# Optimization experiments

Measured on AMD Instinct MI355X. Metric: run time of the kernel, lower is better.

The kernel has to match this reference:

```python
import math
import jax, jax.numpy as jnp
import numpy as np

B, N, D, H = 4, 2048, 512, 8
HD = D // H


def setup_inputs() -> dict:
    key = jax.random.key(0)
    ks = jax.random.split(key, 7)
    w_scale = 1.0 / math.sqrt(D)  # keep logits in a sane range (like default init)
    return {
        "q": jax.random.normal(ks[0], (B, N, D), dtype=jnp.float32),
        "mask": jax.random.randint(ks[1], (B, N), 0, 2) == 1,  # True = masked key
        "attn_bias": jax.random.normal(ks[2], (B, N, N), dtype=jnp.float32),
        "Wq": jax.random.normal(ks[3], (D, D), dtype=jnp.float32) * w_scale,
        "Wk": jax.random.normal(ks[4], (D, D), dtype=jnp.float32) * w_scale,
        "Wv": jax.random.normal(ks[5], (D, D), dtype=jnp.float32) * w_scale,
        "Wo": jax.random.normal(ks[6], (D, D), dtype=jnp.float32) * w_scale,
    }


def _heads(v):
    # [B, N, D] -> [H, B, N, HD]  (mirrors reshape + movedim(-2, 0))
    b, n, d = v.shape
    return v.reshape(b, n, H, HD).transpose(2, 0, 1, 3)


def reference(q, mask, attn_bias, Wq, Wk, Wv, Wo):
    # Linear projections (torch Linear: x @ W.T)
    qh = _heads(q @ Wq.T)
    kh = _heads(q @ Wk.T)   # self-attention: h defaults to q
    vh = _heads(q @ Wv.T)
    # scores: [H, B, Nq, Nk]
    scores = jnp.einsum("hbqd,hbkd->hbqk", qh, kh) / math.sqrt(HD)
    scores = scores + attn_bias[None]                     # broadcast over heads
    scores = jnp.where(mask[None, :, None, :], -jnp.inf, scores)
    attn = jax.nn.softmax(scores, axis=-1)
    out = jnp.einsum("hbqk,hbkd->hbqd", attn, vh)         # [H, B, Nq, HD]
    out = out.transpose(1, 2, 0, 3).reshape(q.shape[0], q.shape[1], D)
    return out @ Wo.T
```

## Files before the change

kernel.cpp:

```cpp
#include <hip/hip_runtime.h>
#include <stdint.h>


typedef __attribute__((ext_vector_type(8))) short short8;
typedef __attribute__((ext_vector_type(4))) short short4v;
typedef __attribute__((ext_vector_type(4))) float f32x4;

#define DEV static __device__ __forceinline__

constexpr int Bc = 4, Nc = 2048, Dc = 512, Hc = 8, HDc = 64;
constexpr int Mc = Bc * Nc;
constexpr int QKVNc = 3 * Dc;

DEV unsigned short f2bits(float f) {
  union { float f; unsigned u; } a; a.f = f;
  unsigned r = a.u + 0x7fffu + ((a.u >> 16) & 1u);
  return (unsigned short)(r >> 16);
}
DEV unsigned pack_bf16x2(float a, float b) {
  unsigned ua = __float_as_uint(a), ub = __float_as_uint(b);
  ua = ua + 0x7fffu + ((ua >> 16) & 1u);
  ub = ub + 0x7fffu + ((ub >> 16) & 1u);
  return __builtin_amdgcn_perm(ub, ua, 0x07060302);
}
DEV unsigned pack_shorts(short a, short b) {
  return (unsigned)(unsigned short)a | ((unsigned)(unsigned short)b << 16);
}

__global__ void cvt_kernel(const float* __restrict__ src, short* __restrict__ dst, int n4) {
  int i = blockIdx.x * blockDim.x + threadIdx.x;
  if (i >= n4) return;
  float4 v = ((const float4*)src)[i];
  short4v o = { (short)f2bits(v.x), (short)f2bits(v.y), (short)f2bits(v.z), (short)f2bits(v.w) };
  ((short4v*)dst)[i] = o;
}

__global__ void detect_kernel(const uchar4* __restrict__ m, int* __restrict__ flag) {
  __shared__ int s;
  if (threadIdx.x == 0) s = 0;
  __syncthreads();
  int acc = 0;
  for (int i = threadIdx.x; i < (Bc * Nc) / 4; i += 256) {
    uchar4 v = m[i];
    acc |= (int)v.y | (int)v.z | (int)v.w;
  }
  if (acc) atomicOr(&s, 1);
  __syncthreads();
  if (threadIdx.x == 0) *flag = s;
}

__global__ void mask_kernel(const void* __restrict__ mask, const int* __restrict__ flag,
                            float* __restrict__ mf, int n) {
  int i = blockIdx.x * blockDim.x + threadIdx.x;
  if (i >= n) return;
  int isbyte = *flag;
  int v = isbyte ? (int)((const unsigned char*)mask)[i] : ((const int*)mask)[i];
  mf[i] = v ? -1e30f : 0.0f;
}

template<bool OUT_F32>
__global__ __launch_bounds__(256) void gemm_bt(const short* __restrict__ A,
                                               const short* __restrict__ Bm,
                                               void* __restrict__ Cv,
                                               int M, int N, int K,
                                               int qcols, float cscale) {
  __shared__ __align__(16) short At[128 * 72];
  __shared__ __align__(16) short Bt[128 * 72];
  const int tid = threadIdx.x, lane = tid & 63, wv = tid >> 6;
  const int quad = lane >> 4, l16 = lane & 15;
  const int mbase = blockIdx.y * 128, nbase = blockIdx.x * 128;
  const int wr = (wv >> 1) * 64, wc = (wv & 1) * 64;
  const float scale = (nbase < qcols) ? cscale : 1.0f;
  const int srow = tid >> 1, sch8 = (tid & 1) * 32;
  (void)srow; (void)sch8;
  f32x4 acc[4][4] = {};
  short8 apre[4], bpre[4];
#pragma unroll
  for (int i = 0; i < 4; i++) {
    int flat = i * 256 + tid, row = flat >> 3, ch8 = (flat & 7) * 8;
    apre[i] = *(const short8*)&A[(size_t)(mbase + row) * K + ch8];
    bpre[i] = *(const short8*)&Bm[(size_t)(nbase + row) * K + ch8];
  }
  for (int k0 = 0; k0 < K; k0 += 64) {
    __syncthreads();
#pragma unroll
    for (int i = 0; i < 4; i++) {
      int flat = i * 256 + tid, row = flat >> 3, ch8 = (flat & 7) * 8;
      *(short8*)&At[row * 72 + ch8] = apre[i];
      *(short8*)&Bt[row * 72 + ch8] = bpre[i];
    }
    if (k0 + 64 < K) {
#pragma unroll
      for (int i = 0; i < 4; i++) {
        int flat = i * 256 + tid, row = flat >> 3, ch8 = (flat & 7) * 8;
        apre[i] = *(const short8*)&A[(size_t)(mbase + row) * K + k0 + 64 + ch8];
        bpre[i] = *(const short8*)&Bm[(size_t)(nbase + row) * K + k0 + 64 + ch8];
      }
    }
    __syncthreads();
#pragma unroll
    for (int s = 0; s < 2; s++) {
      short8 af[4], bf[4];
#pragma unroll
      for (int t = 0; t < 4; t++) {
        af[t] = *(short8*)&At[(wr + t * 16 + l16) * 72 + quad * 8 + s * 32];
        bf[t] = *(short8*)&Bt[(wc + t * 16 + l16) * 72 + quad * 8 + s * 32];
      }
#pragma unroll
      for (int mt = 0; mt < 4; mt++)
#pragma unroll
        for (int nt = 0; nt < 4; nt++)
          acc[mt][nt] = __builtin_amdgcn_mfma_f32_16x16x32_bf16(af[mt], bf[nt], acc[mt][nt], 0, 0, 0);
    }
  }
#pragma unroll
  for (int mt = 0; mt < 4; mt++)
#pragma unroll
    for (int nt = 0; nt < 4; nt++)
#pragma unroll
      for (int r = 0; r < 4; r++) {
        int row = mbase + wr + mt * 16 + quad * 4 + r;
        int col = nbase + wc + nt * 16 + l16;
        float v = acc[mt][nt][r] * scale;
        if (OUT_F32) ((float*)Cv)[(size_t)row * N + col] = v;
        else         ((short*)Cv)[(size_t)row * N + col] = (short)f2bits(v);
      }
}

__global__ __launch_bounds__(256) void attn_kernel(const short* __restrict__ QKV,
                                                   const float* __restrict__ bias,
                                                   const float* __restrict__ maskf,
                                                   short* __restrict__ Aout) {
  __shared__ __align__(16) short Kt[64 * 72];
  __shared__ __align__(16) short Vt[64 * 72];
  __shared__ __align__(16) short Pt[4][16 * 72];
  __shared__ __align__(16) float mlds[Nc];
  __shared__ float lred[4][16];
  const int tid = threadIdx.x, lane = tid & 63, wv = tid >> 6;
  const int quad = lane >> 4, l16 = lane & 15;
  const int qt = blockIdx.x & 31, h = (blockIdx.x >> 5) & 7, b = (int)(blockIdx.x >> 8);
  const int qrow0 = qt * 64;
  const int qglob = qrow0 + wv * 16 + l16;
  const float* biasrow = bias + ((size_t)b * Nc + qglob) * Nc;
  const float* mfb = maskf + b * Nc;

  ((float4*)mlds)[tid]       = ((const float4*)mfb)[tid];
  ((float4*)mlds)[256 + tid] = ((const float4*)mfb)[256 + tid];

  short8 qf[2];
  {
    const short* qp = QKV + (size_t)(b * Nc + qglob) * QKVNc + h * HDc + quad * 8;
    qf[0] = *(const short8*)qp;
    qf[1] = *(const short8*)(qp + 32);
  }

  const int vp = tid & 31, vg = tid >> 5;
  const short* Kbase = QKV + Dc + h * HDc;
  const short* Vbase = QKV + 2 * Dc + h * HDc;

  short8 kpre[2], v0pre, v1pre;
  float4 bpre[4];
#pragma unroll
  for (int i = 0; i < 2; i++) {
    int flat = i * 256 + tid, row = flat >> 3, ch8 = (flat & 7) * 8;
    kpre[i] = *(const short8*)&Kbase[(size_t)(b * Nc + row) * QKVNc + ch8];
  }
  v0pre = *(const short8*)&Vbase[(size_t)(b * Nc + 2 * vp) * QKVNc + vg * 8];
  v1pre = *(const short8*)&Vbase[(size_t)(b * Nc + 2 * vp + 1) * QKVNc + vg * 8];
#pragma unroll
  for (int t = 0; t < 4; t++) bpre[t] = *(const float4*)&biasrow[t * 16 + quad * 4];

  f32x4 oacc[4] = {};
  float lsum = 0.f;

  for (int kt = 0; kt < 32; kt++) {
    const int kb = kt * 64;
    const int kbn = ((kt + 1) & 31) * 64;
    __syncthreads();
#pragma unroll
    for (int i = 0; i < 2; i++) {
      int flat = i * 256 + tid, row = flat >> 3, ch8 = (flat & 7) * 8;
      *(short8*)&Kt[row * 72 + ch8] = kpre[i];
    }
#pragma unroll
    for (int j = 0; j < 8; j++)
      *(unsigned*)&Vt[(vg * 8 + j) * 72 + 2 * vp] = pack_shorts(v0pre[j], v1pre[j]);

    float4 bcur[4];
#pragma unroll
    for (int t = 0; t < 4; t++) bcur[t] = bpre[t];
#pragma unroll
    for (int i = 0; i < 2; i++) {
      int flat = i * 256 + tid, row = flat >> 3, ch8 = (flat & 7) * 8;
      kpre[i] = *(const short8*)&Kbase[(size_t)(b * Nc + kbn + row) * QKVNc + ch8];
    }
    v0pre = *(const short8*)&Vbase[(size_t)(b * Nc + kbn + 2 * vp) * QKVNc + vg * 8];
    v1pre = *(const short8*)&Vbase[(size_t)(b * Nc + kbn + 2 * vp + 1) * QKVNc + vg * 8];
#pragma unroll
    for (int t = 0; t < 4; t++) bpre[t] = *(const float4*)&biasrow[kbn + t * 16 + quad * 4];
    __syncthreads();

    f32x4 sacc[4] = {};
#pragma unroll
    for (int s = 0; s < 2; s++)
#pragma unroll
      for (int t = 0; t < 4; t++) {
        short8 kf = *(short8*)&Kt[(t * 16 + l16) * 72 + quad * 8 + s * 32];
        sacc[t] = __builtin_amdgcn_mfma_f32_16x16x32_bf16(kf, qf[s], sacc[t], 0, 0, 0);
      }

#pragma unroll
    for (int t = 0; t < 4; t++) {
      float4 mv = *(const float4*)&mlds[kb + t * 16 + quad * 4];
      float p0 = __expf(sacc[t][0] + mv.x + bcur[t].x);
      float p1 = __expf(sacc[t][1] + mv.y + bcur[t].y);
      float p2 = __expf(sacc[t][2] + mv.z + bcur[t].z);
      float p3 = __expf(sacc[t][3] + mv.w + bcur[t].w);
      lsum += (p0 + p1) + (p2 + p3);
      uint2 u = { pack_bf16x2(p0, p1), pack_bf16x2(p2, p3) };
      *(uint2*)&Pt[wv][l16 * 72 + t * 16 + quad * 4] = u;
    }

#pragma unroll
    for (int s = 0; s < 2; s++) {
      short8 pf = *(short8*)&Pt[wv][l16 * 72 + quad * 8 + s * 32];
#pragma unroll
      for (int t = 0; t < 4; t++) {
        short8 vf = *(short8*)&Vt[(t * 16 + l16) * 72 + quad * 8 + s * 32];
        oacc[t] = __builtin_amdgcn_mfma_f32_16x16x32_bf16(pf, vf, oacc[t], 0, 0, 0);
      }
    }
  }

  lsum += __shfl_xor(lsum, 16);
  lsum += __shfl_xor(lsum, 32);
  if (quad == 0) lred[wv][l16] = lsum;
#pragma unroll
  for (int r = 0; r < 4; r++) {
    float inv = 1.0f / lred[wv][quad * 4 + r];
    int row = b * Nc + qrow0 + wv * 16 + quad * 4 + r;
#pragma unroll
    for (int t = 0; t < 4; t++)
      Aout[(size_t)row * Dc + h * HDc + t * 16 + l16] = (short)f2bits(oacc[t][r] * inv);
  }
}

extern "C" void kernel_launch(void* const* d_in, const int* in_sizes, int n_in,
                              void* d_out, int out_size, void* d_ws, size_t ws_size,
                              hipStream_t stream) {
  const float* q    = (const float*)d_in[0];
  const void*  mask = d_in[1];
  const float* bias = (const float*)d_in[2];
  const float* Wq   = (const float*)d_in[3];
  const float* Wk   = (const float*)d_in[4];
  const float* Wv   = (const float*)d_in[5];
  const float* Wo   = (const float*)d_in[6];
  float* out = (float*)d_out;

  char* ws = (char*)d_ws;
  short* qb   = (short*)ws;  ws += (size_t)Mc * Dc * 2;
  short* Wqkv = (short*)ws;  ws += (size_t)QKVNc * Dc * 2;
  short* Wob  = (short*)ws;  ws += (size_t)Dc * Dc * 2;
  float* mf   = (float*)ws;  ws += (size_t)Bc * Nc * 4;
  int*   mflag= (int*)ws;    ws += 256;
  short* QKV  = (short*)ws;  ws += (size_t)Mc * QKVNc * 2;
  short* aout = (short*)ws;  ws += (size_t)Mc * Dc * 2;

  auto cvt = [&](const float* s, short* d, int n) {
    int n4 = n >> 2;
    cvt_kernel<<<dim3((n4 + 255) / 256), dim3(256), 0, stream>>>(s, d, n4);
  };
  cvt(q, qb, Mc * Dc);
  cvt(Wq, Wqkv,               Dc * Dc);
  cvt(Wk, Wqkv + Dc * Dc,     Dc * Dc);
  cvt(Wv, Wqkv + 2 * Dc * Dc, Dc * Dc);
  cvt(Wo, Wob, Dc * Dc);
  detect_kernel<<<dim3(1), dim3(256), 0, stream>>>((const uchar4*)mask, mflag);
  mask_kernel<<<dim3((Bc * Nc + 255) / 256), dim3(256), 0, stream>>>(mask, mflag, mf, Bc * Nc);

  gemm_bt<false><<<dim3(QKVNc / 128, Mc / 128), dim3(256), 0, stream>>>(
      qb, Wqkv, (void*)QKV, Mc, QKVNc, Dc, Dc, 0.125f);
  attn_kernel<<<dim3(Bc * Hc * 32), dim3(256), 0, stream>>>(QKV, bias, mf, aout);
  gemm_bt<true><<<dim3(Dc / 128, Mc / 128), dim3(256), 0, stream>>>(
      aout, Wob, (void*)out, Mc, Dc, Dc, 0, 1.0f);
}
```

Baseline: 270.1 us.

## Fuse input conversion into QKV GEMM, merge prep kernels, enlarge attention tiles

The QKV GEMM now reads the fp32 input directly and converts it to bf16 while staging into LDS. This removes the separate conversion kernel and its intermediate buffer. The four weight-conversion launches become one kernel, and the mask detect and mask expand kernels become a single-block kernel, cutting launch count. The attention kernel now uses 512 threads with 128 query rows per block, so each K/V tile loaded into LDS serves twice as many queries. The trade-off is higher register and LDS use per block and fewer blocks in flight.

After: 263.4 us. 1.03x faster.

```diff
diff --git a/kernel.cpp b/kernel.cpp
--- a/kernel.cpp
+++ b/kernel.cpp
@@ -26,44 +26,50 @@
 DEV unsigned pack_shorts(short a, short b) {
   return (unsigned)(unsigned short)a | ((unsigned)(unsigned short)b << 16);
 }
-
-__global__ void cvt_kernel(const float* __restrict__ src, short* __restrict__ dst, int n4) {
-  int i = blockIdx.x * blockDim.x + threadIdx.x;
-  if (i >= n4) return;
-  float4 v = ((const float4*)src)[i];
+DEV short8 cvt8(float4 a, float4 b) {
+  union { short8 s; uint4 u; } r;
+  r.u.x = pack_bf16x2(a.x, a.y); r.u.y = pack_bf16x2(a.z, a.w);
+  r.u.z = pack_bf16x2(b.x, b.y); r.u.w = pack_bf16x2(b.z, b.w);
+  return r.s;
+}
+
+__global__ void cvtw_kernel(const float* __restrict__ Wq, const float* __restrict__ Wk,
+                            const float* __restrict__ Wv, const float* __restrict__ Wo,
+                            short* __restrict__ Wqkv, short* __restrict__ Wob) {
+  int which = blockIdx.x >> 8;
+  int j = (blockIdx.x & 255) * 256 + threadIdx.x;
+  const float* src = which == 0 ? Wq : which == 1 ? Wk : which == 2 ? Wv : Wo;
+  short* dst = (which == 3) ? Wob : Wqkv + which * (Dc * Dc);
+  float4 v = ((const float4*)src)[j];
   short4v o = { (short)f2bits(v.x), (short)f2bits(v.y), (short)f2bits(v.z), (short)f2bits(v.w) };
-  ((short4v*)dst)[i] = o;
-}
-
-__global__ void detect_kernel(const uchar4* __restrict__ m, int* __restrict__ flag) {
-  __shared__ int s;
-  if (threadIdx.x == 0) s = 0;
+  ((short4v*)dst)[j] = o;
+}
+
+__global__ void maskprep_kernel(const void* __restrict__ mask, float* __restrict__ mf) {
+  __shared__ int flag;
+  if (threadIdx.x == 0) flag = 0;
   __syncthreads();
+  const uchar4* m4 = (const uchar4*)mask;
   int acc = 0;
-  for (int i = threadIdx.x; i < (Bc * Nc) / 4; i += 256) {
-    uchar4 v = m[i];
+  for (int i = threadIdx.x; i < 2048; i += 1024) {
+    uchar4 v = m4[i];
     acc |= (int)v.y | (int)v.z | (int)v.w;
   }
-  if (acc) atomicOr(&s, 1);
+  if (acc) atomicOr(&flag, 1);
   __syncthreads();
-  if (threadIdx.x == 0) *flag = s;
-}
-
-__global__ void mask_kernel(const void* __restrict__ mask, const int* __restrict__ flag,
-                            float* __restrict__ mf, int n) {
-  int i = blockIdx.x * blockDim.x + threadIdx.x;
-  if (i >= n) return;
-  int isbyte = *flag;
-  int v = isbyte ? (int)((const unsigned char*)mask)[i] : ((const int*)mask)[i];
-  mf[i] = v ? -1e30f : 0.0f;
-}
-
-template<bool OUT_F32>
-__global__ __launch_bounds__(256) void gemm_bt(const short* __restrict__ A,
-                                               const short* __restrict__ Bm,
-                                               void* __restrict__ Cv,
-                                               int M, int N, int K,
-                                               int qcols, float cscale) {
+  int isbyte = flag;
+  for (int i = threadIdx.x; i < Bc * Nc; i += 1024) {
+    int v = isbyte ? (int)((const unsigned char*)mask)[i] : ((const int*)mask)[i];
+    mf[i] = v ? -1e30f : 0.0f;
+  }
+}
+
+template<bool A_F32, bool OUT_F32>
+__global__ __launch_bounds__(256, 2) void gemm_bt(const void* __restrict__ Av,
+                                                  const short* __restrict__ Bm,
+                                                  void* __restrict__ Cv,
+                                                  int M, int N, int K,
+                                                  int qcols, float cscale) {
   __shared__ __align__(16) short At[128 * 72];
   __shared__ __align__(16) short Bt[128 * 72];
   const int tid = threadIdx.x, lane = tid & 63, wv = tid >> 6;
@@ -71,14 +77,18 @@
   const int mbase = blockIdx.y * 128, nbase = blockIdx.x * 128;
   const int wr = (wv >> 1) * 64, wc = (wv & 1) * 64;
   const float scale = (nbase < qcols) ? cscale : 1.0f;
-  const int srow = tid >> 1, sch8 = (tid & 1) * 32;
-  (void)srow; (void)sch8;
   f32x4 acc[4][4] = {};
-  short8 apre[4], bpre[4];
+  float4 apf[4][2]; short8 aph[4], bpre[4];
 #pragma unroll
   for (int i = 0; i < 4; i++) {
     int flat = i * 256 + tid, row = flat >> 3, ch8 = (flat & 7) * 8;
-    apre[i] = *(const short8*)&A[(size_t)(mbase + row) * K + ch8];
+    if (A_F32) {
+      const float* Af = (const float*)Av;
+      apf[i][0] = *(const float4*)&Af[(size_t)(mbase + row) * K + ch8];
+      apf[i][1] = *(const float4*)&Af[(size_t)(mbase + row) * K + ch8 + 4];
+    } else {
+      aph[i] = *(const short8*)&((const short*)Av)[(size_t)(mbase + row) * K + ch8];
+    }
     bpre[i] = *(const short8*)&Bm[(size_t)(nbase + row) * K + ch8];
   }
   for (int k0 = 0; k0 < K; k0 += 64) {
@@ -86,14 +96,20 @@
 #pragma unroll
     for (int i = 0; i < 4; i++) {
       int flat = i * 256 + tid, row = flat >> 3, ch8 = (flat & 7) * 8;
-      *(short8*)&At[row * 72 + ch8] = apre[i];
+      *(short8*)&At[row * 72 + ch8] = A_F32 ? cvt8(apf[i][0], apf[i][1]) : aph[i];
       *(short8*)&Bt[row * 72 + ch8] = bpre[i];
     }
     if (k0 + 64 < K) {
 #pragma unroll
       for (int i = 0; i < 4; i++) {
         int flat = i * 256 + tid, row = flat >> 3, ch8 = (flat & 7) * 8;
-        apre[i] = *(const short8*)&A[(size_t)(mbase + row) * K + k0 + 64 + ch8];
+        if (A_F32) {
+          const float* Af = (const float*)Av;
+          apf[i][0] = *(const float4*)&Af[(size_t)(mbase + row) * K + k0 + 64 + ch8];
+          apf[i][1] = *(const float4*)&Af[(size_t)(mbase + row) * K + k0 + 64 + ch8 + 4];
+        } else {
+          aph[i] = *(const short8*)&((const short*)Av)[(size_t)(mbase + row) * K + k0 + 64 + ch8];
+        }
         bpre[i] = *(const short8*)&Bm[(size_t)(nbase + row) * K + k0 + 64 + ch8];
       }
     }
@@ -127,25 +143,24 @@
       }
 }
 
-__global__ __launch_bounds__(256) void attn_kernel(const short* __restrict__ QKV,
-                                                   const float* __restrict__ bias,
-                                                   const float* __restrict__ maskf,
-                                                   short* __restrict__ Aout) {
+__global__ __launch_bounds__(512, 3) void attn_kernel(const short* __restrict__ QKV,
+                                                      const float* __restrict__ bias,
+                                                      const float* __restrict__ maskf,
+                                                      short* __restrict__ Aout) {
   __shared__ __align__(16) short Kt[64 * 72];
   __shared__ __align__(16) short Vt[64 * 72];
-  __shared__ __align__(16) short Pt[4][16 * 72];
+  __shared__ __align__(16) short Pt[8][16 * 72];
   __shared__ __align__(16) float mlds[Nc];
-  __shared__ float lred[4][16];
+  __shared__ float lred[8][16];
   const int tid = threadIdx.x, lane = tid & 63, wv = tid >> 6;
   const int quad = lane >> 4, l16 = lane & 15;
-  const int qt = blockIdx.x & 31, h = (blockIdx.x >> 5) & 7, b = (int)(blockIdx.x >> 8);
-  const int qrow0 = qt * 64;
+  const int qt = blockIdx.x & 15, h = (blockIdx.x >> 4) & 7, b = (int)(blockIdx.x >> 7);
+  const int qrow0 = qt * 128;
   const int qglob = qrow0 + wv * 16 + l16;
   const float* biasrow = bias + ((size_t)b * Nc + qglob) * Nc;
   const float* mfb = maskf + b * Nc;
 
-  ((float4*)mlds)[tid]       = ((const float4*)mfb)[tid];
-  ((float4*)mlds)[256 + tid] = ((const float4*)mfb)[256 + tid];
+  ((float4*)mlds)[tid] = ((const float4*)mfb)[tid];
 
   short8 qf[2];
   {
@@ -154,19 +169,15 @@
     qf[1] = *(const short8*)(qp + 32);
   }
 
-  const int vp = tid & 31, vg = tid >> 5;
+  const int vp = tid & 31, vq = tid >> 5;
+  const int krow = tid >> 3, kch = (tid & 7) * 8;
   const short* Kbase = QKV + Dc + h * HDc;
   const short* Vbase = QKV + 2 * Dc + h * HDc;
 
-  short8 kpre[2], v0pre, v1pre;
-  float4 bpre[4];
-#pragma unroll
-  for (int i = 0; i < 2; i++) {
-    int flat = i * 256 + tid, row = flat >> 3, ch8 = (flat & 7) * 8;
-    kpre[i] = *(const short8*)&Kbase[(size_t)(b * Nc + row) * QKVNc + ch8];
-  }
-  v0pre = *(const short8*)&Vbase[(size_t)(b * Nc + 2 * vp) * QKVNc + vg * 8];
-  v1pre = *(const short8*)&Vbase[(size_t)(b * Nc + 2 * vp + 1) * QKVNc + vg * 8];
+  short8 kpre; short4v v0pre, v1pre; float4 bpre[4];
+  kpre  = *(const short8*)&Kbase[(size_t)(b * Nc + krow) * QKVNc + kch];
+  v0pre = *(const short4v*)&Vbase[(size_t)(b * Nc + 2 * vp) * QKVNc + 4 * vq];
+  v1pre = *(const short4v*)&Vbase[(size_t)(b * Nc + 2 * vp + 1) * QKVNc + 4 * vq];
 #pragma unroll
   for (int t = 0; t < 4; t++) bpre[t] = *(const float4*)&biasrow[t * 16 + quad * 4];
 
@@ -177,25 +188,17 @@
     const int kb = kt * 64;
     const int kbn = ((kt + 1) & 31) * 64;
     __syncthreads();
-#pragma unroll
-    for (int i = 0; i < 2; i++) {
-      int flat = i * 256 + tid, row = flat >> 3, ch8 = (flat & 7) * 8;
-      *(short8*)&Kt[row * 72 + ch8] = kpre[i];
-    }
-#pragma unroll
-    for (int j = 0; j < 8; j++)
-      *(unsigned*)&Vt[(vg * 8 + j) * 72 + 2 * vp] = pack_shorts(v0pre[j], v1pre[j]);
+    *(short8*)&Kt[krow * 72 + kch] = kpre;
+#pragma unroll
+    for (int j = 0; j < 4; j++)
+      *(unsigned*)&Vt[(4 * vq + j) * 72 + 2 * vp] = pack_shorts(v0pre[j], v1pre[j]);
 
     float4 bcur[4];
 #pragma unroll
     for (int t = 0; t < 4; t++) bcur[t] = bpre[t];
-#pragma unroll
-    for (int i = 0; i < 2; i++) {
-      int flat = i * 256 + tid, row = flat >> 3, ch8 = (flat & 7) * 8;
-      kpre[i] = *(const short8*)&Kbase[(size_t)(b * Nc + kbn + row) * QKVNc + ch8];
-    }
-    v0pre = *(const short8*)&Vbase[(size_t)(b * Nc + kbn + 2 * vp) * QKVNc + vg * 8];
-    v1pre = *(const short8*)&Vbase[(size_t)(b * Nc + kbn + 2 * vp + 1) * QKVNc + vg * 8];
+    kpre  = *(const short8*)&Kbase[(size_t)(b * Nc + kbn + krow) * QKVNc + kch];
+    v0pre = *(const short4v*)&Vbase[(size_t)(b * Nc + kbn + 2 * vp) * QKVNc + 4 * vq];
+    v1pre = *(const short4v*)&Vbase[(size_t)(b * Nc + kbn + 2 * vp + 1) * QKVNc + 4 * vq];
 #pragma unroll
     for (int t = 0; t < 4; t++) bpre[t] = *(const float4*)&biasrow[kbn + t * 16 + quad * 4];
     __syncthreads();
@@ -258,29 +261,18 @@
   float* out = (float*)d_out;
 
   char* ws = (char*)d_ws;
-  short* qb   = (short*)ws;  ws += (size_t)Mc * Dc * 2;
   short* Wqkv = (short*)ws;  ws += (size_t)QKVNc * Dc * 2;
   short* Wob  = (short*)ws;  ws += (size_t)Dc * Dc * 2;
   float* mf   = (float*)ws;  ws += (size_t)Bc * Nc * 4;
-  int*   mflag= (int*)ws;    ws += 256;
   short* QKV  = (short*)ws;  ws += (size_t)Mc * QKVNc * 2;
   short* aout = (short*)ws;  ws += (size_t)Mc * Dc * 2;
 
-  auto cvt = [&](const float* s, short* d, int n) {
-    int n4 = n >> 2;
-    cvt_kernel<<<dim3((n4 + 255) / 256), dim3(256), 0, stream>>>(s, d, n4);
-  };
-  cvt(q, qb, Mc * Dc);
-  cvt(Wq, Wqkv,               Dc * Dc);
-  cvt(Wk, Wqkv + Dc * Dc,     Dc * Dc);
-  cvt(Wv, Wqkv + 2 * Dc * Dc, Dc * Dc);
-  cvt(Wo, Wob, Dc * Dc);
-  detect_kernel<<<dim3(1), dim3(256), 0, stream>>>((const uchar4*)mask, mflag);
-  mask_kernel<<<dim3((Bc * Nc + 255) / 256), dim3(256), 0, stream>>>(mask, mflag, mf, Bc * Nc);
-
-  gemm_bt<false><<<dim3(QKVNc / 128, Mc / 128), dim3(256), 0, stream>>>(
-      qb, Wqkv, (void*)QKV, Mc, QKVNc, Dc, Dc, 0.125f);
-  attn_kernel<<<dim3(Bc * Hc * 32), dim3(256), 0, stream>>>(QKV, bias, mf, aout);
-  gemm_bt<true><<<dim3(Dc / 128, Mc / 128), dim3(256), 0, stream>>>(
-      aout, Wob, (void*)out, Mc, Dc, Dc, 0, 1.0f);
-}
+  cvtw_kernel<<<dim3(1024), dim3(256), 0, stream>>>(Wq, Wk, Wv, Wo, Wqkv, Wob);
+  maskprep_kernel<<<dim3(1), dim3(1024), 0, stream>>>(mask, mf);
+
+  gemm_bt<true, false><<<dim3(QKVNc / 128, Mc / 128), dim3(256), 0, stream>>>(
+      (const void*)q, Wqkv, (void*)QKV, Mc, QKVNc, Dc, Dc, 0.125f);
+  attn_kernel<<<dim3(Bc * Hc * 16), dim3(512), 0, stream>>>(QKV, bias, mf, aout);
+  gemm_bt<false, true><<<dim3(Dc / 128, Mc / 128), dim3(256), 0, stream>>>(
+      (const void*)aout, Wob, (void*)out, Mc, Dc, Dc, 0, 1.0f);
+}
```
